# Optimization experiments

Measured on AMD Instinct MI355X. Metric: run time of the kernel, lower is better.

The kernel has to match this reference:

```python
import jax, jax.numpy as jnp
import numpy as np
from jax import lax

H = 128; NOISE = 128; L = 16; A = 10; HYB = 3; F_NODE = 17; E_FEAT = 4
TEMP = 1.0
MAX_VALENCES = jnp.array([4., 3., 2., 1., 4., 2., 6., 1., 4., 4.], dtype=jnp.float32)


def setup_inputs():
    key = jax.random.key(0)
    ks = jax.random.split(key, 16)
    B, N = 4096, 32
    def w(k, *s):
        return jax.random.normal(k, s, dtype=jnp.float32) * 0.05
    return {
        'noise': jax.random.normal(ks[0], (B, NOISE), dtype=jnp.float32),
        'w1': w(ks[1], NOISE, H), 'b1': jnp.zeros((H,), jnp.float32),
        'gat_w': w(ks[2], L, H, H), 'gat_b': jnp.zeros((L, H), jnp.float32),
        'att_src': w(ks[3], L, H), 'att_dst': w(ks[4], L, H),
        'w_atom': w(ks[5], H, A), 'b_atom': jnp.zeros((A,), jnp.float32),
        'w_hyb': w(ks[6], H, HYB), 'b_hyb': jnp.zeros((HYB,), jnp.float32),
        'w_deg': w(ks[7], H, 1), 'b_deg': jnp.zeros((1,), jnp.float32),
        'w_chg': w(ks[8], H, 1), 'b_chg': jnp.zeros((1,), jnp.float32),
        'w_arom': w(ks[9], H, 1), 'b_arom': jnp.zeros((1,), jnp.float32),
        'w_eex': w(ks[10], 2 * F_NODE, 1), 'b_eex': jnp.zeros((1,), jnp.float32),
        'w_ety': w(ks[11], 2 * F_NODE, E_FEAT), 'b_ety': jnp.zeros((E_FEAT,), jnp.float32),
        'batch_size': B, 'num_nodes': N,
    }


def _gumbel(k, shape):
    u = jax.random.uniform(k, shape, minval=1e-6, maxval=1.0 - 1e-6)
    return -jnp.log(-jnp.log(u))


def reference(noise, w1, b1, gat_w, gat_b, att_src, att_dst, w_atom, b_atom,
              w_hyb, b_hyb, w_deg, b_deg, w_chg, b_chg, w_arom, b_arom,
              w_eex, b_eex, w_ety, b_ety, batch_size, num_nodes):
    B, N = batch_size, num_nodes
    h0 = jax.nn.relu(noise @ w1 + b1)                      # [B,H]
    x = jnp.broadcast_to(h0[:, None, :], (B, N, h0.shape[-1]))
    idx = jnp.arange(N)
    # chain adjacency (both directions) + self loops (PyG GATConv default)
    adj = (jnp.abs(idx[:, None] - idx[None, :]) == 1) | (idx[:, None] == idx[None, :])
    neg = jnp.float32(-1e9)

    def layer(xc, p):
        W, b, a_s, a_d = p
        h = xc @ W + b                                     # [B,N,H]
        e_src = h @ a_s                                    # [B,N]
        e_dst = h @ a_d
        s = jax.nn.leaky_relu(e_dst[:, :, None] + e_src[:, None, :], 0.2)  # [B,N,N]
        s = jnp.where(adj, s, neg)
        alpha = jax.nn.softmax(s, axis=-1)
        out = jnp.einsum('bij,bjh->bih', alpha, h)
        return jax.nn.relu(out + xc), None                 # residual GAT layer

    x, _ = lax.scan(layer, x, (gat_w, gat_b, att_src, att_dst))

    sk = jax.random.split(jax.random.key(42), 4)
    # atom type head + categorical sampling (Gumbel-max on logits/T)
    atom_logits = x @ w_atom + b_atom                      # [B,N,A]
    atom_lp = jax.nn.log_softmax(atom_logits, axis=-1)
    atom_idx = jnp.argmax(atom_logits / TEMP + _gumbel(sk[0], atom_logits.shape), axis=-1)
    atom_lp_mol = jnp.take_along_axis(atom_lp, atom_idx[..., None], axis=-1)[..., 0].mean(axis=1)
    # hybridization head
    hyb_logits = x @ w_hyb + b_hyb                         # [B,N,3]
    hyb_lp = jax.nn.log_softmax(hyb_logits, axis=-1)
    hyb_idx = jnp.argmax(hyb_logits / TEMP + _gumbel(sk[1], hyb_logits.shape), axis=-1)
    hyb_lp_mol = jnp.take_along_axis(hyb_lp, hyb_idx[..., None], axis=-1)[..., 0].mean(axis=1)
    # remaining node heads
    deg = jax.nn.sigmoid(x @ w_deg + b_deg)
    chg = jnp.tanh(lax.stop_gradient(x @ w_chg + b_chg))   # .clone().detach() in torch
    arom_p = jax.nn.sigmoid(x @ w_arom + b_arom)
    arom = (jax.random.uniform(sk[2], arom_p.shape) < arom_p).astype(jnp.float32)
    val = (MAX_VALENCES[atom_idx] / 5.0)[..., None]
    node_features = jnp.concatenate([
        jax.nn.one_hot(atom_idx, A, dtype=jnp.float32), deg, chg,
        jax.nn.one_hot(hyb_idx, HYB, dtype=jnp.float32), arom, val], axis=-1)  # [B,N,17]
    # edge heads on chain edges (both directions)
    u = jnp.arange(N - 1); v = u + 1
    eu = jnp.concatenate([u, v]); ev = jnp.concatenate([v, u])
    ef = jnp.concatenate([node_features[:, eu], node_features[:, ev]], axis=-1)  # [B,2(N-1),34]
    exist_p = jax.nn.sigmoid(ef @ w_eex + b_eex)[..., 0]
    edge_mask = exist_p > 0.5
    type_logits = ef @ w_ety + b_ety
    type_idx = jnp.argmax(type_logits / TEMP + _gumbel(sk[3], type_logits.shape), axis=-1)
    edge_attr = jax.nn.one_hot(type_idx, E_FEAT, dtype=jnp.float32)
    return node_features, atom_lp_mol, hyb_lp_mol, edge_attr, edge_mask
```

## Files before the change

kernel.cpp:

```cpp
#include <hip/hip_runtime.h>
#include <stdint.h>
#include <math.h>


typedef double d4 __attribute__((ext_vector_type(4)));

struct U2 { uint32_t a, b; };

__device__ __forceinline__ U2 threefry(uint32_t k0, uint32_t k1, uint32_t x0, uint32_t x1) {
  const uint32_t ks2 = k0 ^ k1 ^ 0x1BD11BDAu;
#define TFR(r) { x0 += x1; x1 = (x1 << (r)) | (x1 >> (32 - (r))); x1 ^= x0; }
  x0 += k0;  x1 += k1;
  TFR(13) TFR(15) TFR(26) TFR(6)
  x0 += k1;  x1 += ks2 + 1u;
  TFR(17) TFR(29) TFR(16) TFR(24)
  x0 += ks2; x1 += k0 + 2u;
  TFR(13) TFR(15) TFR(26) TFR(6)
  x0 += k0;  x1 += k1 + 3u;
  TFR(17) TFR(29) TFR(16) TFR(24)
  x0 += k1;  x1 += ks2 + 4u;
  TFR(13) TFR(15) TFR(26) TFR(6)
  x0 += ks2; x1 += k0 + 5u;
#undef TFR
  U2 r; r.a = x0; r.b = x1; return r;
}

__device__ __forceinline__ uint32_t pbits(uint32_t k0, uint32_t k1, uint32_t ctr) {
  U2 r = threefry(k0, k1, 0u, ctr);
  return r.a ^ r.b;
}

__device__ __forceinline__ float bits_to_unit(uint32_t bits) {
  return __uint_as_float((bits >> 9) | 0x3f800000u) - 1.0f;
}

__device__ __forceinline__ float jgumbel(uint32_t k0, uint32_t k1, uint32_t ctr) {
  const float minv = 1e-6f;
  const float maxv = (float)(1.0 - 1e-6);
  const float span = maxv - minv;
  float f = bits_to_unit(pbits(k0, k1, ctr));
  float u = fmaxf(minv, __fadd_rn(__fmul_rn(f, span), minv));
  return -logf(-logf(u));
}

extern "C" __global__ void __launch_bounds__(512)
gen_kernel(const float* __restrict__ noise,
           const float* __restrict__ w1,
           const float* __restrict__ b1,
           const float* __restrict__ gat_w,
           const float* __restrict__ gat_b,
           const float* __restrict__ w_atom,
           const float* __restrict__ b_atom,
           const float* __restrict__ w_hyb,
           const float* __restrict__ b_hyb,
           const float* __restrict__ w_deg,
           const float* __restrict__ b_deg,
           const float* __restrict__ w_chg,
           const float* __restrict__ b_chg,
           const float* __restrict__ w_arom,
           const float* __restrict__ b_arom,
           const float* __restrict__ w_eex,
           const float* __restrict__ b_eex,
           const float* __restrict__ w_ety,
           const float* __restrict__ b_ety,
           float* __restrict__ out)
{
  __shared__ __align__(16) double sX[2][128][18];
  __shared__ double sScr[16][16];
  __shared__ float  sNF[16][32][17];
  __shared__ double sLP[16][64];

  const int t       = threadIdx.x;
  const int wv      = t >> 6;
  const int ln      = t & 63;
  const int g       = ln >> 4;
  const int i       = ln & 15;
  const int molBase = blockIdx.x * 16;
  const int colb    = wv << 4;

  int rowOf[4], colOf[4];
  {
    d4 z4 = {0.0, 0.0, 0.0, 0.0};
    const double selK0 = (g == 0) ? 1.0 : 0.0;
    const double idxv  = (double)i;
    d4 prow = __builtin_amdgcn_mfma_f64_16x16x4f64(idxv,  selK0, z4, 0, 0, 0);
    d4 pcol = __builtin_amdgcn_mfma_f64_16x16x4f64(selK0, idxv,  z4, 0, 0, 0);
    #pragma unroll
    for (int j = 0; j < 4; ++j) {
      rowOf[j] = (int)prow[j];
      colOf[j] = (int)pcol[j];
    }
  }

  float wr0[32], wr1[32];

  #pragma unroll
  for (int ks = 0; ks < 32; ++ks)
    wr0[ks] = w1[(((ks << 2) + g) << 7) + colb + i];

  #pragma unroll
  for (int it = 0; it < 4; ++it) {
    const int idx = t + (it << 9);
    const int c = idx & 127, m = idx >> 7;
    sX[0][c][m] = (double)noise[(((size_t)(molBase + m)) << 7) + c];
  }
  __syncthreads();

  int p = 0;

#define LAYERSTEP(WUSE, WPRE, nextWptr, bptr, ISFIRST)                          \
  {                                                                             \
    const int q = p ^ 1;                                                        \
    const float* __restrict__ nW = (nextWptr);                                  \
    _Pragma("unroll")                                                           \
    for (int ks = 0; ks < 32; ++ks)                                             \
      WPRE[ks] = nW[(((ks << 2) + g) << 7) + colb + i];                         \
    d4 ac0 = {0.0,0.0,0.0,0.0}, ac1 = {0.0,0.0,0.0,0.0};                        \
    d4 ac2 = {0.0,0.0,0.0,0.0}, ac3 = {0.0,0.0,0.0,0.0};                        \
    _Pragma("unroll")                                                           \
    for (int ks = 0; ks < 32; ks += 4) {                                        \
      ac0 = __builtin_amdgcn_mfma_f64_16x16x4f64(sX[p][((ks + 0) << 2) + g][i], \
            (double)WUSE[ks + 0], ac0, 0, 0, 0);                                \
      ac1 = __builtin_amdgcn_mfma_f64_16x16x4f64(sX[p][((ks + 1) << 2) + g][i], \
            (double)WUSE[ks + 1], ac1, 0, 0, 0);                                \
      ac2 = __builtin_amdgcn_mfma_f64_16x16x4f64(sX[p][((ks + 2) << 2) + g][i], \
            (double)WUSE[ks + 2], ac2, 0, 0, 0);                                \
      ac3 = __builtin_amdgcn_mfma_f64_16x16x4f64(sX[p][((ks + 3) << 2) + g][i], \
            (double)WUSE[ks + 3], ac3, 0, 0, 0);                                \
    }                                                                           \
    _Pragma("unroll")                                                           \
    for (int j = 0; j < 4; ++j) {                                               \
      const int cc = colb + colOf[j];                                           \
      double tv = ((ac0[j] + ac1[j]) + (ac2[j] + ac3[j])) + (double)(bptr)[cc]; \
      if (!(ISFIRST)) tv += sX[p][cc][rowOf[j]];                                \
      sX[q][cc][rowOf[j]] = fmax(tv, 0.0);                                      \
    }                                                                           \
    __syncthreads();                                                            \
    p = q;                                                                      \
  }

  LAYERSTEP(wr0, wr1, gat_w, b1, 1)

  #pragma unroll 1
  for (int li = 0; li < 8; ++li) {
    const int lA = 2 * li;
    const int lB = 2 * li + 1;
    const int pfA = lB;
    const int pfB = (lB + 1 < 16) ? (lB + 1) : 15;
    LAYERSTEP(wr1, wr0, gat_w + ((size_t)pfA << 14), gat_b + (lA << 7), 0)
    LAYERSTEP(wr0, wr1, gat_w + ((size_t)pfB << 14), gat_b + (lB << 7), 0)
  }
#undef LAYERSTEP

  if (t < 256) {
    const int mh = t >> 4;
    const int h  = t & 15;
    const float* wp; int stride; double bias;
    if (h < 10)       { wp = w_atom + h;        stride = 10; bias = (double)b_atom[h]; }
    else if (h < 13)  { wp = w_hyb + (h - 10);  stride = 3;  bias = (double)b_hyb[h - 10]; }
    else if (h == 13) { wp = w_deg;             stride = 1;  bias = (double)b_deg[0]; }
    else if (h == 14) { wp = w_chg;             stride = 1;  bias = (double)b_chg[0]; }
    else              { wp = w_arom;            stride = 1;  bias = (double)b_arom[0]; }
    double acc = 0.0;
    for (int c = 0; c < 128; ++c)
      acc = fma(sX[p][c][mh], (double)wp[c * stride], acc);
    sScr[mh][h] = acc + bias;
  }
  __syncthreads();

  const U2 k0p = threefry(0u, 42u, 0u, 0u);
  const U2 k1p = threefry(0u, 42u, 0u, 1u);
  const U2 k2p = threefry(0u, 42u, 0u, 2u);
  const U2 k3p = threefry(0u, 42u, 0u, 3u);

  {
    const int mloc = t >> 5;
    const int n    = t & 31;
    const int mol  = molBase + mloc;
    const double* scr = sScr[mloc];

    double m = scr[0];
    #pragma unroll
    for (int a = 1; a < 10; ++a) m = fmax(m, scr[a]);
    double lsum = 0.0;
    #pragma unroll
    for (int a = 0; a < 10; ++a) lsum += exp(scr[a] - m);
    const double lse = log(lsum);
    const uint32_t abase = ((uint32_t)mol * 32u + (uint32_t)n) * 10u;
    int asel = 0; double abest = 0.0;
    #pragma unroll
    for (int a = 0; a < 10; ++a) {
      const double gg = (double)jgumbel(k0p.a, k0p.b, abase + (uint32_t)a);
      const double sc = scr[a] + gg;
      if (a == 0 || sc > abest) { abest = sc; asel = a; }
    }
    sLP[mloc][n] = (scr[asel] - m) - lse;

    double m2 = fmax(fmax(scr[10], scr[11]), scr[12]);
    double ls2 = exp(scr[10] - m2) + exp(scr[11] - m2) + exp(scr[12] - m2);
    const double lse2 = log(ls2);
    const uint32_t hbase = ((uint32_t)mol * 32u + (uint32_t)n) * 3u;
    int hsel = 0; double hbest = 0.0;
    #pragma unroll
    for (int j = 0; j < 3; ++j) {
      const double gg = (double)jgumbel(k1p.a, k1p.b, hbase + (uint32_t)j);
      const double sc = scr[10 + j] + gg;
      if (j == 0 || sc > hbest) { hbest = sc; hsel = j; }
    }
    sLP[mloc][32 + n] = (scr[10 + hsel] - m2) - lse2;

    const double deg = 1.0 / (1.0 + exp(-scr[13]));
    const double chg = tanh(scr[14]);
    const double pr  = 1.0 / (1.0 + exp(-scr[15]));
    const uint32_t ridx = (uint32_t)mol * 32u + (uint32_t)n;
    const double uu = (double)bits_to_unit(pbits(k2p.a, k2p.b, ridx));
    const double arom = (uu < pr) ? 1.0 : 0.0;
    const double valt[10] = {4.0/5.0, 3.0/5.0, 2.0/5.0, 1.0/5.0, 4.0/5.0,
                             2.0/5.0, 6.0/5.0, 1.0/5.0, 4.0/5.0, 4.0/5.0};
    double nf[17];
    #pragma unroll
    for (int q2 = 0; q2 < 10; ++q2) nf[q2] = (q2 == asel) ? 1.0 : 0.0;
    nf[10] = deg; nf[11] = chg;
    #pragma unroll
    for (int j = 0; j < 3; ++j) nf[12 + j] = (j == hsel) ? 1.0 : 0.0;
    nf[15] = arom; nf[16] = valt[asel];

    const size_t o = ((size_t)mol * 32 + n) * 17;
    #pragma unroll
    for (int q2 = 0; q2 < 17; ++q2) {
      sNF[mloc][n][q2] = (float)nf[q2];
      out[o + q2] = (float)nf[q2];
    }
  }
  __syncthreads();

  #pragma unroll 1
  for (int r = 0; r < 2; ++r) {
    const int mloc = (r << 3) + wv;
    const int mol  = molBase + mloc;
    if (ln == 62) {
      double sa = 0.0;
      for (int n = 0; n < 32; ++n) sa += sLP[mloc][n];
      out[2228224 + (size_t)mol] = (float)(sa / 32.0);
    } else if (ln == 63) {
      double sh = 0.0;
      for (int n = 0; n < 32; ++n) sh += sLP[mloc][32 + n];
      out[2232320 + (size_t)mol] = (float)(sh / 32.0);
    } else {
      const int e = ln;
      const int nu_ = (e < 31) ? e : (e - 30);
      const int nv_ = (e < 31) ? (e + 1) : (e - 31);
      double lex = 0.0;
      double lt[4] = {0.0, 0.0, 0.0, 0.0};
      for (int q2 = 0; q2 < 17; ++q2) {
        const double f = (double)sNF[mloc][nu_][q2];
        lex = fma(f, (double)w_eex[q2], lex);
        #pragma unroll
        for (int c = 0; c < 4; ++c) lt[c] = fma(f, (double)w_ety[q2 * 4 + c], lt[c]);
      }
      for (int q2 = 0; q2 < 17; ++q2) {
        const double f = (double)sNF[mloc][nv_][q2];
        lex = fma(f, (double)w_eex[17 + q2], lex);
        #pragma unroll
        for (int c = 0; c < 4; ++c) lt[c] = fma(f, (double)w_ety[(17 + q2) * 4 + c], lt[c]);
      }
      lex += (double)b_eex[0];
      #pragma unroll
      for (int c = 0; c < 4; ++c) lt[c] += (double)b_ety[c];

      const double pex = 1.0 / (1.0 + exp(-lex));
      out[3252224 + (size_t)mol * 62 + e] = (pex > 0.5) ? 1.f : 0.f;

      const uint32_t tbase = ((uint32_t)mol * 62u + (uint32_t)e) * 4u;
      int tsel = 0; double tbest = 0.0;
      #pragma unroll
      for (int c = 0; c < 4; ++c) {
        const double gg = (double)jgumbel(k3p.a, k3p.b, tbase + (uint32_t)c);
        const double sc = lt[c] + gg;
        if (c == 0 || sc > tbest) { tbest = sc; tsel = c; }
      }
      const size_t o = 2236416 + ((size_t)mol * 62 + e) * 4;
      #pragma unroll
      for (int c = 0; c < 4; ++c) out[o + c] = (c == tsel) ? 1.f : 0.f;
    }
  }
}

extern "C" void kernel_launch(void* const* d_in, const int* in_sizes, int n_in,
                              void* d_out, int out_size, void* d_ws, size_t ws_size,
                              hipStream_t stream) {
  (void)in_sizes; (void)n_in; (void)out_size; (void)d_ws; (void)ws_size;
  hipLaunchKernelGGL(gen_kernel, dim3(256), dim3(512), 0, stream,
                     (const float*)d_in[0],  (const float*)d_in[1],
                     (const float*)d_in[2],  (const float*)d_in[3],
                     (const float*)d_in[4],
                     (const float*)d_in[7],  (const float*)d_in[8],
                     (const float*)d_in[9],  (const float*)d_in[10],
                     (const float*)d_in[11], (const float*)d_in[12],
                     (const float*)d_in[13], (const float*)d_in[14],
                     (const float*)d_in[15], (const float*)d_in[16],
                     (const float*)d_in[17], (const float*)d_in[18],
                     (const float*)d_in[19], (const float*)d_in[20],
                     (float*)d_out);
}
```

Before: 177.9 us.

## Split GEMM K dimension across wave pairs with LDS reduction, doubling block size

Doubles the block to 1024 threads so each output column tile is computed by two waves, each handling half of the K dimension. The partial MFMA accumulators are combined through a new shared-memory reduction buffer before the bias, residual and ReLU are applied. This halves the serial MFMA chain and the weight registers per wave, aiming to cut per-layer latency with only 256 blocks available. In exchange it adds an extra barrier and an LDS round trip per layer, and most threads sit idle in the later epilogue stages.

```diff
diff --git a/kernel.cpp b/kernel.cpp
--- a/kernel.cpp
+++ b/kernel.cpp
@@ -43,7 +43,7 @@
   return -logf(-logf(u));
 }
 
-extern "C" __global__ void __launch_bounds__(512)
+extern "C" __global__ void __launch_bounds__(1024)
 gen_kernel(const float* __restrict__ noise,
            const float* __restrict__ w1,
            const float* __restrict__ b1,
@@ -66,6 +66,7 @@
            float* __restrict__ out)
 {
   __shared__ __align__(16) double sX[2][128][18];
+  __shared__ __align__(16) double sRed[8][64][4];
   __shared__ double sScr[16][16];
   __shared__ float  sNF[16][32][17];
   __shared__ double sLP[16][64];
@@ -76,7 +77,9 @@
   const int g       = ln >> 4;
   const int i       = ln & 15;
   const int molBase = blockIdx.x * 16;
-  const int colb    = wv << 4;
+  const int colt    = wv >> 1;
+  const int wh      = wv & 1;
+  const int colb    = colt << 4;
 
   int rowOf[4], colOf[4];
   {
@@ -92,15 +95,15 @@
     }
   }
 
-  float wr0[32], wr1[32];
+  float wr0[16], wr1[16];
 
   #pragma unroll
-  for (int ks = 0; ks < 32; ++ks)
-    wr0[ks] = w1[(((ks << 2) + g) << 7) + colb + i];
+  for (int ks = 0; ks < 16; ++ks)
+    wr0[ks] = w1[((((wh << 4) + ks) << 2) + g) * 128 + colb + i];
 
   #pragma unroll
-  for (int it = 0; it < 4; ++it) {
-    const int idx = t + (it << 9);
+  for (int it = 0; it < 2; ++it) {
+    const int idx = t + (it << 10);
     const int c = idx & 127, m = idx >> 7;
     sX[0][c][m] = (double)noise[(((size_t)(molBase + m)) << 7) + c];
   }
@@ -113,27 +116,34 @@
     const int q = p ^ 1;                                                        \
     const float* __restrict__ nW = (nextWptr);                                  \
     _Pragma("unroll")                                                           \
-    for (int ks = 0; ks < 32; ++ks)                                             \
-      WPRE[ks] = nW[(((ks << 2) + g) << 7) + colb + i];                         \
+    for (int ks = 0; ks < 16; ++ks)                                             \
+      WPRE[ks] = nW[((((wh << 4) + ks) << 2) + g) * 128 + colb + i];            \
     d4 ac0 = {0.0,0.0,0.0,0.0}, ac1 = {0.0,0.0,0.0,0.0};                        \
-    d4 ac2 = {0.0,0.0,0.0,0.0}, ac3 = {0.0,0.0,0.0,0.0};                        \
     _Pragma("unroll")                                                           \
-    for (int ks = 0; ks < 32; ks += 4) {                                        \
-      ac0 = __builtin_amdgcn_mfma_f64_16x16x4f64(sX[p][((ks + 0) << 2) + g][i], \
-            (double)WUSE[ks + 0], ac0, 0, 0, 0);                                \
-      ac1 = __builtin_amdgcn_mfma_f64_16x16x4f64(sX[p][((ks + 1) << 2) + g][i], \
-            (double)WUSE[ks + 1], ac1, 0, 0, 0);                                \
-      ac2 = __builtin_amdgcn_mfma_f64_16x16x4f64(sX[p][((ks + 2) << 2) + g][i], \
-            (double)WUSE[ks + 2], ac2, 0, 0, 0);                                \
-      ac3 = __builtin_amdgcn_mfma_f64_16x16x4f64(sX[p][((ks + 3) << 2) + g][i], \
-            (double)WUSE[ks + 3], ac3, 0, 0, 0);                                \
+    for (int ks = 0; ks < 16; ks += 2) {                                        \
+      ac0 = __builtin_amdgcn_mfma_f64_16x16x4f64(                               \
+              sX[p][(((wh << 4) + ks)     << 2) + g][i],                        \
+              (double)WUSE[ks],     ac0, 0, 0, 0);                              \
+      ac1 = __builtin_amdgcn_mfma_f64_16x16x4f64(                               \
+              sX[p][(((wh << 4) + ks + 1) << 2) + g][i],                        \
+              (double)WUSE[ks + 1], ac1, 0, 0, 0);                              \
     }                                                                           \
-    _Pragma("unroll")                                                           \
-    for (int j = 0; j < 4; ++j) {                                               \
-      const int cc = colb + colOf[j];                                           \
-      double tv = ((ac0[j] + ac1[j]) + (ac2[j] + ac3[j])) + (double)(bptr)[cc]; \
-      if (!(ISFIRST)) tv += sX[p][cc][rowOf[j]];                                \
-      sX[q][cc][rowOf[j]] = fmax(tv, 0.0);                                      \
+    if (wh == 1) {                                                              \
+      double2 v;                                                                \
+      v.x = ac0[0] + ac1[0]; v.y = ac0[1] + ac1[1];                             \
+      *(double2*)&sRed[colt][ln][0] = v;                                        \
+      v.x = ac0[2] + ac1[2]; v.y = ac0[3] + ac1[3];                             \
+      *(double2*)&sRed[colt][ln][2] = v;                                        \
+    }                                                                           \
+    __syncthreads();                                                            \
+    if (wh == 0) {                                                              \
+      _Pragma("unroll")                                                         \
+      for (int j = 0; j < 4; ++j) {                                             \
+        const int cc = colb + colOf[j];                                         \
+        double tv = (ac0[j] + ac1[j]) + sRed[colt][ln][j] + (double)(bptr)[cc]; \
+        if (!(ISFIRST)) tv += sX[p][cc][rowOf[j]];                              \
+        sX[q][cc][rowOf[j]] = fmax(tv, 0.0);                                    \
+      }                                                                         \
     }                                                                           \
     __syncthreads();                                                            \
     p = q;                                                                      \
@@ -173,7 +183,7 @@
   const U2 k2p = threefry(0u, 42u, 0u, 2u);
   const U2 k3p = threefry(0u, 42u, 0u, 3u);
 
-  {
+  if (t < 512) {
     const int mloc = t >> 5;
     const int n    = t & 31;
     const int mol  = molBase + mloc;
@@ -234,9 +244,8 @@
   }
   __syncthreads();
 
-  #pragma unroll 1
-  for (int r = 0; r < 2; ++r) {
-    const int mloc = (r << 3) + wv;
+  {
+    const int mloc = wv;
     const int mol  = molBase + mloc;
     if (ln == 62) {
       double sa = 0.0;
@@ -290,7 +299,7 @@
                               void* d_out, int out_size, void* d_ws, size_t ws_size,
                               hipStream_t stream) {
   (void)in_sizes; (void)n_in; (void)out_size; (void)d_ws; (void)ws_size;
-  hipLaunchKernelGGL(gen_kernel, dim3(256), dim3(512), 0, stream,
+  hipLaunchKernelGGL(gen_kernel, dim3(256), dim3(1024), 0, stream,
                      (const float*)d_in[0],  (const float*)d_in[1],
                      (const float*)d_in[2],  (const float*)d_in[3],
                      (const float*)d_in[4],
```

Result: slower. 183.3 us (+3.0%).
